# Performance work log

Hardware: AMD Instinct MI355X
Metric: run time of the kernel (lower is better)

## Reference

```python
import jax, jax.numpy as jnp
import numpy as np

N, D, FF, T = 131072, 128, 512, 4
EPS = 1e-5


def layernorm(x, g, b):
    m = jnp.mean(x, axis=-1, keepdims=True)
    v = jnp.mean((x - m) ** 2, axis=-1, keepdims=True)
    return (x - m) * jax.lax.rsqrt(v + EPS) * g + b


def setup_inputs() -> dict:
    key = jax.random.key(0)
    ks = jax.random.split(key, 12)
    s = 1.0 / np.sqrt(D)
    return {
        "x": jax.random.normal(ks[0], (N, D), dtype=jnp.float32),
        # attention projections (single head; nhead=1 is forced by the source's shape constraints)
        "Kw": jax.random.normal(ks[1], (D, D), dtype=jnp.float32) * s,
        "Qw": jax.random.normal(ks[2], (D, D), dtype=jnp.float32) * s,
        "Vw": jax.random.normal(ks[3], (D, D), dtype=jnp.float32) * s,
        "ln1_g": jnp.ones((D,), jnp.float32),
        "ln1_b": jnp.zeros((D,), jnp.float32),
        "ln2_g": jnp.ones((D,), jnp.float32),
        "ln2_b": jnp.zeros((D,), jnp.float32),
        "w1": jax.random.normal(ks[4], (D, FF), dtype=jnp.float32) * s,
        "b1": jnp.zeros((FF,), jnp.float32),
        "w2": jax.random.normal(ks[5], (FF, D), dtype=jnp.float32) / np.sqrt(FF),
        "b2": jnp.zeros((D,), jnp.float32),
        "out_w": jax.random.normal(ks[6], (D, D), dtype=jnp.float32) * s,
        "out_b": jnp.zeros((D,), jnp.float32),
    }


def reference(x, Kw, Qw, Vw, ln1_g, ln1_b, ln2_g, ln2_b, w1, b1, w2, b2, out_w, out_b):
    for _ in range(T):  # same params reused every timestep, as in the source
        # --- softmax-free attention sublayer ---
        h = layernorm(x, ln1_g, ln1_b)
        Q = h @ Qw
        K = h @ Kw
        V = h @ Vw
        # (Q @ K^T) @ V == Q @ (K^T @ V): no softmax, so reassociate to O(n*d^2)
        x = x + Q @ (K.T @ V)
        # --- feed-forward sublayer (Linear-ReLU-Linear implied by dim_ff) ---
        h = layernorm(x, ln2_g, ln2_b)
        x = x + (jax.nn.relu(h @ w1 + b1) @ w2 + b2)
    return x @ out_w + out_b
```

## Files before the change

### kernel.cpp

```cpp
#include <hip/hip_runtime.h>

#define NROWS 131072
#define DIM   128
#define FFD   512
#define TSTEPS 4
#define NBLK  512
#define CHUNK 128
#define NCHUNK 2
#define NSLOT 16
#define SH    136

static_assert((long)NBLK * CHUNK * NCHUNK == NROWS, "grid/chunk mismatch");

typedef short          s8v   __attribute__((ext_vector_type(8)));
typedef float          f4v   __attribute__((ext_vector_type(4)));
typedef unsigned short u16x4 __attribute__((ext_vector_type(4)));

#define MFMA16(a,b,c) __builtin_amdgcn_mfma_f32_16x16x32_bf16((a),(b),(c),0,0,0)

__device__ __forceinline__ unsigned short f2bf(float f){
    unsigned u = __builtin_bit_cast(unsigned, f);
    u += 0x7FFFu + ((u >> 16) & 1u);
    return (unsigned short)(u >> 16);
}
__device__ __forceinline__ float bf2f(unsigned short h){
    return __builtin_bit_cast(float, (unsigned)h << 16);
}
__device__ __forceinline__ f4v ntload4(const float* p){
    return __builtin_nontemporal_load((const f4v*)p);
}
__device__ __forceinline__ void ntstore4(float* p, f4v v){
    __builtin_nontemporal_store(v, (f4v*)p);
}

__global__ __launch_bounds__(512, 2)
void kA(const float* __restrict__ x, const unsigned short* __restrict__ Kwp,
        const unsigned short* __restrict__ Vwp,
        const float* __restrict__ ga, const float* __restrict__ be,
        float* __restrict__ slots)
{
    __shared__ unsigned short hh[128*SH];
    __shared__ unsigned short hl[128*SH];
    __shared__ unsigned short KT[128*SH];
    __shared__ unsigned short VT[128*SH];
    const int tid  = threadIdx.x;
    const int wv   = tid >> 6, lane = tid & 63;
    const int quad = lane >> 4, l15 = lane & 15;
    const int lp   = lane >> 3, lr = lane & 7;
    const int myrow = wv*8 + lr;
    const int pc    = wv*16 + l15;

    s8v bfK[4], bfV[4];
    #pragma unroll
    for (int ks = 0; ks < 4; ++ks) {
        bfK[ks] = *(const s8v*)(Kwp + pc*DIM + ks*32 + quad*8);
        bfV[ks] = *(const s8v*)(Vwp + pc*DIM + ks*32 + quad*8);
    }

    f4v acc[8];
    #pragma unroll
    for (int i = 0; i < 8; ++i) acc[i] = (f4v){0.f,0.f,0.f,0.f};

    for (int ch = 0; ch < NCHUNK; ++ch) {
        const size_t r0 = ((size_t)blockIdx.x*NCHUNK + ch)*CHUNK;
        #pragma unroll
        for (int pp = 0; pp < 2; ++pp) {
            const int row = pp*64 + myrow;
            float v[16];
            #pragma unroll
            for (int j = 0; j < 4; ++j) {
                const f4v t = ntload4(x + (r0 + row)*DIM + lp*16 + j*4);
                v[j*4+0] = t[0]; v[j*4+1] = t[1]; v[j*4+2] = t[2]; v[j*4+3] = t[3];
            }
            float s = 0.f, q = 0.f;
            #pragma unroll
            for (int i = 0; i < 16; ++i) { s += v[i]; q += v[i]*v[i]; }
            #pragma unroll
            for (int o = 8; o < 64; o <<= 1) { s += __shfl_xor(s, o); q += __shfl_xor(q, o); }
            const float m  = s * (1.0f/128.0f);
            const float rs = rsqrtf(q * (1.0f/128.0f) - m*m + 1e-5f);
            unsigned short hi16[16], lo16[16];
            #pragma unroll
            for (int j = 0; j < 4; ++j) {
                const float4 g = *(const float4*)(ga + lp*16 + j*4);
                const float4 b = *(const float4*)(be + lp*16 + j*4);
                float hv0 = (v[j*4+0]-m)*rs*g.x + b.x;
                float hv1 = (v[j*4+1]-m)*rs*g.y + b.y;
                float hv2 = (v[j*4+2]-m)*rs*g.z + b.z;
                float hv3 = (v[j*4+3]-m)*rs*g.w + b.w;
                hi16[j*4+0] = f2bf(hv0); lo16[j*4+0] = f2bf(hv0 - bf2f(hi16[j*4+0]));
                hi16[j*4+1] = f2bf(hv1); lo16[j*4+1] = f2bf(hv1 - bf2f(hi16[j*4+1]));
                hi16[j*4+2] = f2bf(hv2); lo16[j*4+2] = f2bf(hv2 - bf2f(hi16[j*4+2]));
                hi16[j*4+3] = f2bf(hv3); lo16[j*4+3] = f2bf(hv3 - bf2f(hi16[j*4+3]));
            }
            #pragma unroll
            for (int j = 0; j < 2; ++j) {
                *(s8v*)&hh[row*SH + lp*16 + j*8] = *(const s8v*)&hi16[j*8];
                *(s8v*)&hl[row*SH + lp*16 + j*8] = *(const s8v*)&lo16[j*8];
            }
        }
        __syncthreads();
        #pragma unroll
        for (int p = 0; p < 2; ++p) {
            const s8v* bf = p ? bfV : bfK;
            unsigned short* T = p ? VT : KT;
            #pragma unroll
            for (int mt = 0; mt < 8; ++mt) {
                s8v ah[4], al[4];
                #pragma unroll
                for (int ks = 0; ks < 4; ++ks) {
                    ah[ks] = *(const s8v*)(&hh[(mt*16 + l15)*SH + ks*32 + quad*8]);
                    al[ks] = *(const s8v*)(&hl[(mt*16 + l15)*SH + ks*32 + quad*8]);
                }
                f4v c = {0.f,0.f,0.f,0.f};
                #pragma unroll
                for (int ks = 0; ks < 4; ++ks) c = MFMA16(ah[ks], bf[ks], c);
                #pragma unroll
                for (int ks = 0; ks < 4; ++ks) c = MFMA16(al[ks], bf[ks], c);
                u16x4 w4 = { f2bf(c[0]), f2bf(c[1]), f2bf(c[2]), f2bf(c[3]) };
                *(u16x4*)&T[pc*SH + mt*16 + quad*4] = w4;
            }
        }
        __syncthreads();
        #pragma unroll
        for (int ks = 0; ks < 4; ++ks) {
            const s8v af = *(const s8v*)(&KT[pc*SH + ks*32 + quad*8]);
            #pragma unroll
            for (int jt = 0; jt < 8; ++jt) {
                const s8v bfr = *(const s8v*)(&VT[(jt*16 + l15)*SH + ks*32 + quad*8]);
                acc[jt] = MFMA16(af, bfr, acc[jt]);
            }
        }
        __syncthreads();
    }
    float* S = slots + (size_t)(blockIdx.x & (NSLOT-1)) * 16384;
    #pragma unroll
    for (int jt = 0; jt < 8; ++jt) {
        const int i0 = wv*16 + quad*4;
        const int j  = jt*16 + l15;
        #pragma unroll
        for (int rg = 0; rg < 4; ++rg)
            atomicAdd(&S[(i0 + rg)*DIM + j], acc[jt][rg]);
    }
}

__global__ void kReduce(const float* __restrict__ slots, float* __restrict__ ktv)
{
    const int e = blockIdx.x*256 + threadIdx.x;
    float s = 0.f;
    #pragma unroll
    for (int b = 0; b < NSLOT; ++b) s += slots[(size_t)b*16384 + e];
    ktv[e] = s;
}

__global__ void kBuildM(const float* __restrict__ Qw, const float* __restrict__ ktv,
                        unsigned short* __restrict__ Mp, unsigned short* __restrict__ Ml)
{
    const int idx = blockIdx.x*256 + threadIdx.x;
    const int j = idx >> 7, k = idx & 127;
    float s = 0.f;
    for (int i = 0; i < 128; ++i) s += Qw[k*128 + i] * ktv[i*128 + j];
    const unsigned short hi = f2bf(s);
    Mp[idx] = hi;
    Ml[idx] = f2bf(s - bf2f(hi));
}

__global__ __launch_bounds__(512, 2)
void kB(const float* __restrict__ xin, float* __restrict__ xout,
        const unsigned short* __restrict__ Mp, const unsigned short* __restrict__ Ml,
        const float* __restrict__ g1a, const float* __restrict__ b1a,
        const float* __restrict__ g2a, const float* __restrict__ b2a,
        const unsigned short* __restrict__ w1p, const float* __restrict__ fb1,
        const unsigned short* __restrict__ w2p, const float* __restrict__ fb2)
{
    __shared__ float          xb[128*132];
    __shared__ unsigned short hs[128*SH];
    __shared__ unsigned short fbuf[128*SH];
    unsigned short* const hl = fbuf;
    const int tid  = threadIdx.x;
    const int wv   = tid >> 6, lane = tid & 63;
    const int quad = lane >> 4, l15 = lane & 15;
    const int lp   = lane >> 3, lr = lane & 7;
    const int myrow = wv*8 + lr;
    const int cg    = wv*16 + l15;

    s8v bh[4], bl[4];
    #pragma unroll
    for (int ks = 0; ks < 4; ++ks) {
        bh[ks] = *(const s8v*)(Mp + cg*DIM + ks*32 + quad*8);
        bl[ks] = *(const s8v*)(Ml + cg*DIM + ks*32 + quad*8);
    }

    for (int ch = 0; ch < NCHUNK; ++ch) {
        const size_t r0 = ((size_t)blockIdx.x*NCHUNK + ch)*CHUNK;
        #pragma unroll
        for (int i = 0; i < 8; ++i) {
            const int idx = tid + i*512;
            const int r = idx >> 5, c = (idx & 31)*4;
            const f4v t = ntload4(xin + (r0 + r)*DIM + c);
            *(f4v*)&xb[r*132 + c] = t;
        }
        __syncthreads();
        #pragma unroll
        for (int pp = 0; pp < 2; ++pp) {
            const int row = pp*64 + myrow;
            float v[16];
            #pragma unroll
            for (int j = 0; j < 4; ++j)
                *(float4*)&v[j*4] = *(const float4*)&xb[row*132 + lp*16 + j*4];
            float s = 0.f, q = 0.f;
            #pragma unroll
            for (int i = 0; i < 16; ++i) { s += v[i]; q += v[i]*v[i]; }
            #pragma unroll
            for (int o = 8; o < 64; o <<= 1) { s += __shfl_xor(s, o); q += __shfl_xor(q, o); }
            const float m  = s * (1.0f/128.0f);
            const float rs = rsqrtf(q * (1.0f/128.0f) - m*m + 1e-5f);
            unsigned short hi16[16], lo16[16];
            #pragma unroll
            for (int j = 0; j < 4; ++j) {
                const float4 g = *(const float4*)(g1a + lp*16 + j*4);
                const float4 b = *(const float4*)(b1a + lp*16 + j*4);
                float hv0 = (v[j*4+0]-m)*rs*g.x + b.x;
                float hv1 = (v[j*4+1]-m)*rs*g.y + b.y;
                float hv2 = (v[j*4+2]-m)*rs*g.z + b.z;
                float hv3 = (v[j*4+3]-m)*rs*g.w + b.w;
                hi16[j*4+0] = f2bf(hv0); lo16[j*4+0] = f2bf(hv0 - bf2f(hi16[j*4+0]));
                hi16[j*4+1] = f2bf(hv1); lo16[j*4+1] = f2bf(hv1 - bf2f(hi16[j*4+1]));
                hi16[j*4+2] = f2bf(hv2); lo16[j*4+2] = f2bf(hv2 - bf2f(hi16[j*4+2]));
                hi16[j*4+3] = f2bf(hv3); lo16[j*4+3] = f2bf(hv3 - bf2f(hi16[j*4+3]));
            }
            #pragma unroll
            for (int j = 0; j < 2; ++j) {
                *(s8v*)&hs[row*SH + lp*16 + j*8] = *(const s8v*)&hi16[j*8];
                *(s8v*)&hl[row*SH + lp*16 + j*8] = *(const s8v*)&lo16[j*8];
            }
        }
        __syncthreads();
        #pragma unroll
        for (int mt = 0; mt < 8; ++mt) {
            s8v ah[4], al[4];
            #pragma unroll
            for (int ks = 0; ks < 4; ++ks) {
                ah[ks] = *(const s8v*)(&hs[(mt*16 + l15)*SH + ks*32 + quad*8]);
                al[ks] = *(const s8v*)(&hl[(mt*16 + l15)*SH + ks*32 + quad*8]);
            }
            f4v c = {0.f,0.f,0.f,0.f};
            #pragma unroll
            for (int ks = 0; ks < 4; ++ks) c = MFMA16(ah[ks], bh[ks], c);
            #pragma unroll
            for (int ks = 0; ks < 4; ++ks) c = MFMA16(ah[ks], bl[ks], c);
            #pragma unroll
            for (int ks = 0; ks < 4; ++ks) c = MFMA16(al[ks], bh[ks], c);
            #pragma unroll
            for (int rg = 0; rg < 4; ++rg)
                xb[(mt*16 + quad*4 + rg)*132 + cg] += c[rg];
        }
        __syncthreads();
        #pragma unroll
        for (int pp = 0; pp < 2; ++pp) {
            const int row = pp*64 + myrow;
            float v[16];
            #pragma unroll
            for (int j = 0; j < 4; ++j)
                *(float4*)&v[j*4] = *(const float4*)&xb[row*132 + lp*16 + j*4];
            float s = 0.f, q = 0.f;
            #pragma unroll
            for (int i = 0; i < 16; ++i) { s += v[i]; q += v[i]*v[i]; }
            #pragma unroll
            for (int o = 8; o < 64; o <<= 1) { s += __shfl_xor(s, o); q += __shfl_xor(q, o); }
            const float m  = s * (1.0f/128.0f);
            const float rs = rsqrtf(q * (1.0f/128.0f) - m*m + 1e-5f);
            unsigned short hi16[16];
            #pragma unroll
            for (int j = 0; j < 4; ++j) {
                const float4 g = *(const float4*)(g2a + lp*16 + j*4);
                const float4 b = *(const float4*)(b2a + lp*16 + j*4);
                hi16[j*4+0] = f2bf((v[j*4+0]-m)*rs*g.x + b.x);
                hi16[j*4+1] = f2bf((v[j*4+1]-m)*rs*g.y + b.y);
                hi16[j*4+2] = f2bf((v[j*4+2]-m)*rs*g.z + b.z);
                hi16[j*4+3] = f2bf((v[j*4+3]-m)*rs*g.w + b.w);
            }
            #pragma unroll
            for (int j = 0; j < 2; ++j)
                *(s8v*)&hs[row*SH + lp*16 + j*8] = *(const s8v*)&hi16[j*8];
        }
        __syncthreads();
        f4v dx2[8];
        #pragma unroll
        for (int i = 0; i < 8; ++i) dx2[i] = (f4v){0.f,0.f,0.f,0.f};
        #pragma unroll
        for (int qf = 0; qf < 4; ++qf) {
            const int ffc = qf*128 + cg;
            s8v wa[4];
            #pragma unroll
            for (int ks = 0; ks < 4; ++ks)
                wa[ks] = *(const s8v*)(w1p + ffc*DIM + ks*32 + quad*8);
            const float bias = fb1[ffc];
            #pragma unroll
            for (int mt = 0; mt < 8; ++mt) {
                s8v af[4];
                #pragma unroll
                for (int ks = 0; ks < 4; ++ks)
                    af[ks] = *(const s8v*)(&hs[(mt*16 + l15)*SH + ks*32 + quad*8]);
                f4v c = {0.f,0.f,0.f,0.f};
                #pragma unroll
                for (int ks = 0; ks < 4; ++ks) c = MFMA16(af[ks], wa[ks], c);
                #pragma unroll
                for (int rg = 0; rg < 4; ++rg) {
                    float vv = c[rg] + bias;
                    vv = vv > 0.f ? vv : 0.f;
                    fbuf[(mt*16 + quad*4 + rg)*SH + cg] = f2bf(vv);
                }
            }
            __syncthreads();
            s8v wb[4];
            #pragma unroll
            for (int ks = 0; ks < 4; ++ks)
                wb[ks] = *(const s8v*)(w2p + cg*FFD + qf*128 + ks*32 + quad*8);
            #pragma unroll
            for (int mt = 0; mt < 8; ++mt) {
                s8v af[4];
                #pragma unroll
                for (int ks = 0; ks < 4; ++ks)
                    af[ks] = *(const s8v*)(&fbuf[(mt*16 + l15)*SH + ks*32 + quad*8]);
                f4v c = dx2[mt];
                #pragma unroll
                for (int ks = 0; ks < 4; ++ks) c = MFMA16(af[ks], wb[ks], c);
                dx2[mt] = c;
            }
            __syncthreads();
        }
        {
            const float bias = fb2[cg];
            #pragma unroll
            for (int mt = 0; mt < 8; ++mt)
                #pragma unroll
                for (int rg = 0; rg < 4; ++rg)
                    xb[(mt*16 + quad*4 + rg)*132 + cg] += dx2[mt][rg] + bias;
        }
        __syncthreads();
        #pragma unroll
        for (int i = 0; i < 8; ++i) {
            const int idx = tid + i*512;
            const int r = idx >> 5, c = (idx & 31)*4;
            ntstore4(xout + (r0 + r)*DIM + c, *(const f4v*)&xb[r*132 + c]);
        }
        __syncthreads();
    }
}

#define CHUNKF 64
#define NCHUNKF 4
static_assert((long)NBLK * CHUNKF * NCHUNKF == NROWS, "kF grid mismatch");

__global__ __launch_bounds__(256, 2)
void kF(const float* __restrict__ x, const unsigned short* __restrict__ Owp,
        const float* __restrict__ ob, float* __restrict__ out)
{
    __shared__ unsigned short hh[64*SH];
    __shared__ unsigned short hl[64*SH];
    __shared__ float          xb[64*132];
    const int tid  = threadIdx.x;
    const int quad = (tid & 63) >> 4, l15 = tid & 15;
    const int wv_  = tid >> 6;

    s8v bf[2][4];
    #pragma unroll
    for (int nt = 0; nt < 2; ++nt)
        #pragma unroll
        for (int ks = 0; ks < 4; ++ks)
            bf[nt][ks] = *(const s8v*)(Owp + (wv_*32 + nt*16 + l15)*DIM + ks*32 + quad*8);

    for (int ch = 0; ch < NCHUNKF; ++ch) {
        const size_t r0 = ((size_t)blockIdx.x*NCHUNKF + ch)*CHUNKF;
        #pragma unroll
        for (int i = 0; i < 8; ++i) {
            const int idx = tid + i*256;
            const int r = idx >> 5, c = (idx & 31)*4;
            const f4v v = ntload4(x + (r0 + r)*DIM + c);
            const unsigned short h0 = f2bf(v[0]), h1 = f2bf(v[1]),
                                 h2 = f2bf(v[2]), h3 = f2bf(v[3]);
            u16x4 w4 = { h0, h1, h2, h3 };
            u16x4 l4 = { f2bf(v[0] - bf2f(h0)), f2bf(v[1] - bf2f(h1)),
                         f2bf(v[2] - bf2f(h2)), f2bf(v[3] - bf2f(h3)) };
            *(u16x4*)&hh[r*SH + c] = w4;
            *(u16x4*)&hl[r*SH + c] = l4;
        }
        __syncthreads();
        #pragma unroll
        for (int mt = 0; mt < 4; ++mt) {
            s8v ah[4], al[4];
            #pragma unroll
            for (int ks = 0; ks < 4; ++ks) {
                ah[ks] = *(const s8v*)(&hh[(mt*16 + l15)*SH + ks*32 + quad*8]);
                al[ks] = *(const s8v*)(&hl[(mt*16 + l15)*SH + ks*32 + quad*8]);
            }
            #pragma unroll
            for (int nt = 0; nt < 2; ++nt) {
                f4v c = {0.f,0.f,0.f,0.f};
                #pragma unroll
                for (int ks = 0; ks < 4; ++ks) c = MFMA16(ah[ks], bf[nt][ks], c);
                #pragma unroll
                for (int ks = 0; ks < 4; ++ks) c = MFMA16(al[ks], bf[nt][ks], c);
                const int cg = wv_*32 + nt*16 + l15;
                const float bias = ob[cg];
                #pragma unroll
                for (int rg = 0; rg < 4; ++rg)
                    xb[(mt*16 + quad*4 + rg)*132 + cg] = c[rg] + bias;
            }
        }
        __syncthreads();
        #pragma unroll
        for (int i = 0; i < 8; ++i) {
            const int idx = tid + i*256;
            const int r = idx >> 5, c = (idx & 31)*4;
            ntstore4(out + (r0 + r)*DIM + c, *(const f4v*)&xb[r*132 + c]);
        }
        __syncthreads();
    }
}

__global__ void kPack(const float* __restrict__ Kw, const float* __restrict__ Vw,
                      const float* __restrict__ Ow, const float* __restrict__ w1,
                      const float* __restrict__ w2,
                      unsigned short* __restrict__ Kwp, unsigned short* __restrict__ Vwp,
                      unsigned short* __restrict__ Owp, unsigned short* __restrict__ w1p,
                      unsigned short* __restrict__ w2p)
{
    const int t = blockIdx.x*256 + threadIdx.x;
    if (t < 16384) {
        const int n = t >> 7, k = t & 127;
        Kwp[t] = f2bf(Kw[k*128 + n]);
        Vwp[t] = f2bf(Vw[k*128 + n]);
        Owp[t] = f2bf(Ow[k*128 + n]);
    } else if (t < 16384 + 65536) {
        const int u = t - 16384;
        const int n = u >> 7, k = u & 127;
        w1p[u] = f2bf(w1[k*FFD + n]);
    } else {
        const int u = t - 16384 - 65536;
        const int n = u >> 9, k = u & 511;
        w2p[u] = f2bf(w2[k*DIM + n]);
    }
}

extern "C" void kernel_launch(void* const* d_in, const int* in_sizes, int n_in,
                              void* d_out, int out_size, void* d_ws, size_t ws_size,
                              hipStream_t stream)
{
    (void)in_sizes; (void)n_in; (void)out_size; (void)ws_size;
    const float* x_in = (const float*)d_in[0];
    const float* Kw   = (const float*)d_in[1];
    const float* Qw   = (const float*)d_in[2];
    const float* Vw   = (const float*)d_in[3];
    const float* ln1g = (const float*)d_in[4];
    const float* ln1b = (const float*)d_in[5];
    const float* ln2g = (const float*)d_in[6];
    const float* ln2b = (const float*)d_in[7];
    const float* w1   = (const float*)d_in[8];
    const float* b1   = (const float*)d_in[9];
    const float* w2   = (const float*)d_in[10];
    const float* b2   = (const float*)d_in[11];
    const float* Ow   = (const float*)d_in[12];
    const float* ob   = (const float*)d_in[13];

    char* p = (char*)d_ws;
    float* slots        = (float*)p;          p += (size_t)NSLOT*16384*4;
    float* ktv          = (float*)p;          p += 16384*4;
    unsigned short* Kwp = (unsigned short*)p; p += 16384*2;
    unsigned short* Vwp = (unsigned short*)p; p += 16384*2;
    unsigned short* Owp = (unsigned short*)p; p += 16384*2;
    unsigned short* w1p = (unsigned short*)p; p += 65536*2;
    unsigned short* w2p = (unsigned short*)p; p += 65536*2;
    unsigned short* Mp  = (unsigned short*)p; p += 16384*2;
    unsigned short* Ml  = (unsigned short*)p; p += 16384*2;

    float* X = (float*)d_out;

    kPack<<<576, 256, 0, stream>>>(Kw, Vw, Ow, w1, w2, Kwp, Vwp, Owp, w1p, w2p);

    const float* src = x_in;
    for (int t = 0; t < TSTEPS; ++t) {
        hipMemsetAsync(slots, 0, (size_t)NSLOT*16384*4, stream);
        kA<<<NBLK, 512, 0, stream>>>(src, Kwp, Vwp, ln1g, ln1b, slots);
        kReduce<<<64, 256, 0, stream>>>(slots, ktv);
        kBuildM<<<64, 256, 0, stream>>>(Qw, ktv, Mp, Ml);
        kB<<<NBLK, 512, 0, stream>>>(src, X, Mp, Ml, ln1g, ln1b, ln2g, ln2b,
                                     w1p, b1, w2p, b2);
        src = X;
    }
    kF<<<NBLK, 256, 0, stream>>>(X, Owp, ob, (float*)d_out);
}
```

Measured before the change: 1.195 ms.

## Fuse next-step K^T·V accumulation into block kernel and final projection into last step

The per-row block kernel now does two more things after writing the updated x. It recomputes LayerNorm1 on the rows it already holds in LDS, projects them through K and V with MFMA, and accumulates the next timestep's K^T·V into the slot buffer with atomics. This removes the separate kA pass, and its full read of x, for steps 2 to 4. The last timestep uses a separate variant that applies the output projection directly, which removes the standalone kF pass. In exchange, LDS is aliased across more phases, the per-block epilogue gets longer, and more register pressure is added from the persistent accumulators.

```diff
diff --git a/kernel.cpp b/kernel.cpp
--- a/kernel.cpp
+++ b/kernel.cpp
@@ -166,17 +166,23 @@
 }
 
 __global__ __launch_bounds__(512, 2)
-void kB(const float* __restrict__ xin, float* __restrict__ xout,
-        const unsigned short* __restrict__ Mp, const unsigned short* __restrict__ Ml,
-        const float* __restrict__ g1a, const float* __restrict__ b1a,
-        const float* __restrict__ g2a, const float* __restrict__ b2a,
-        const unsigned short* __restrict__ w1p, const float* __restrict__ fb1,
-        const unsigned short* __restrict__ w2p, const float* __restrict__ fb2)
+void kBmid(const float* __restrict__ xin, float* __restrict__ xout,
+           const unsigned short* __restrict__ Mp, const unsigned short* __restrict__ Ml,
+           const float* __restrict__ g1a, const float* __restrict__ b1a,
+           const float* __restrict__ g2a, const float* __restrict__ b2a,
+           const unsigned short* __restrict__ w1p, const float* __restrict__ fb1,
+           const unsigned short* __restrict__ w2p, const float* __restrict__ fb2,
+           const unsigned short* __restrict__ Kwp, const unsigned short* __restrict__ Vwp,
+           float* __restrict__ slots)
 {
-    __shared__ float          xb[128*132];
-    __shared__ unsigned short hs[128*SH];
-    __shared__ unsigned short fbuf[128*SH];
-    unsigned short* const hl = fbuf;
+    __shared__ __align__(16) char lds_raw[139264];
+    unsigned short* const hs = (unsigned short*)lds_raw;
+    unsigned short* const hl = (unsigned short*)(lds_raw + 34816);
+    float*          const xb = (float*)(lds_raw + 69632);
+    unsigned short* const KT = (unsigned short*)(lds_raw + 69632);
+    unsigned short* const VT = (unsigned short*)(lds_raw + 104448);
+    unsigned short* const fbuf = hl;
+
     const int tid  = threadIdx.x;
     const int wv   = tid >> 6, lane = tid & 63;
     const int quad = lane >> 4, l15 = lane & 15;
@@ -184,12 +190,9 @@
     const int myrow = wv*8 + lr;
     const int cg    = wv*16 + l15;
 
-    s8v bh[4], bl[4];
+    f4v acc[8];
     #pragma unroll
-    for (int ks = 0; ks < 4; ++ks) {
-        bh[ks] = *(const s8v*)(Mp + cg*DIM + ks*32 + quad*8);
-        bl[ks] = *(const s8v*)(Ml + cg*DIM + ks*32 + quad*8);
-    }
+    for (int i = 0; i < 8; ++i) acc[i] = (f4v){0.f,0.f,0.f,0.f};
 
     for (int ch = 0; ch < NCHUNK; ++ch) {
         const size_t r0 = ((size_t)blockIdx.x*NCHUNK + ch)*CHUNK;
@@ -236,24 +239,32 @@
             }
         }
         __syncthreads();
-        #pragma unroll
-        for (int mt = 0; mt < 8; ++mt) {
-            s8v ah[4], al[4];
+        {
+            s8v bh[4], bl[4];
             #pragma unroll
             for (int ks = 0; ks < 4; ++ks) {
-                ah[ks] = *(const s8v*)(&hs[(mt*16 + l15)*SH + ks*32 + quad*8]);
-                al[ks] = *(const s8v*)(&hl[(mt*16 + l15)*SH + ks*32 + quad*8]);
-            }
-            f4v c = {0.f,0.f,0.f,0.f};
-            #pragma unroll
-            for (int ks = 0; ks < 4; ++ks) c = MFMA16(ah[ks], bh[ks], c);
-            #pragma unroll
-            for (int ks = 0; ks < 4; ++ks) c = MFMA16(ah[ks], bl[ks], c);
-            #pragma unroll
-            for (int ks = 0; ks < 4; ++ks) c = MFMA16(al[ks], bh[ks], c);
-            #pragma unroll
-            for (int rg = 0; rg < 4; ++rg)
-                xb[(mt*16 + quad*4 + rg)*132 + cg] += c[rg];
+                bh[ks] = *(const s8v*)(Mp + cg*DIM + ks*32 + quad*8);
+                bl[ks] = *(const s8v*)(Ml + cg*DIM + ks*32 + quad*8);
+            }
+            #pragma unroll
+            for (int mt = 0; mt < 8; ++mt) {
+                s8v ah[4], al[4];
+                #pragma unroll
+                for (int ks = 0; ks < 4; ++ks) {
+                    ah[ks] = *(const s8v*)(&hs[(mt*16 + l15)*SH + ks*32 + quad*8]);
+                    al[ks] = *(const s8v*)(&hl[(mt*16 + l15)*SH + ks*32 + quad*8]);
+                }
+                f4v c = {0.f,0.f,0.f,0.f};
+                #pragma unroll
+                for (int ks = 0; ks < 4; ++ks) c = MFMA16(ah[ks], bh[ks], c);
+                #pragma unroll
+                for (int ks = 0; ks < 4; ++ks) c = MFMA16(ah[ks], bl[ks], c);
+                #pragma unroll
+                for (int ks = 0; ks < 4; ++ks) c = MFMA16(al[ks], bh[ks], c);
+                #pragma unroll
+                for (int rg = 0; rg < 4; ++rg)
+                    xb[(mt*16 + quad*4 + rg)*132 + cg] += c[rg];
+            }
         }
         __syncthreads();
         #pragma unroll
@@ -345,65 +356,303 @@
             const int r = idx >> 5, c = (idx & 31)*4;
             ntstore4(xout + (r0 + r)*DIM + c, *(const f4v*)&xb[r*132 + c]);
         }
+        #pragma unroll
+        for (int pp = 0; pp < 2; ++pp) {
+            const int row = pp*64 + myrow;
+            float v[16];
+            #pragma unroll
+            for (int j = 0; j < 4; ++j)
+                *(float4*)&v[j*4] = *(const float4*)&xb[row*132 + lp*16 + j*4];
+            float s = 0.f, q = 0.f;
+            #pragma unroll
+            for (int i = 0; i < 16; ++i) { s += v[i]; q += v[i]*v[i]; }
+            #pragma unroll
+            for (int o = 8; o < 64; o <<= 1) { s += __shfl_xor(s, o); q += __shfl_xor(q, o); }
+            const float m  = s * (1.0f/128.0f);
+            const float rs = rsqrtf(q * (1.0f/128.0f) - m*m + 1e-5f);
+            unsigned short hi16[16], lo16[16];
+            #pragma unroll
+            for (int j = 0; j < 4; ++j) {
+                const float4 g = *(const float4*)(g1a + lp*16 + j*4);
+                const float4 b = *(const float4*)(b1a + lp*16 + j*4);
+                float hv0 = (v[j*4+0]-m)*rs*g.x + b.x;
+                float hv1 = (v[j*4+1]-m)*rs*g.y + b.y;
+                float hv2 = (v[j*4+2]-m)*rs*g.z + b.z;
+                float hv3 = (v[j*4+3]-m)*rs*g.w + b.w;
+                hi16[j*4+0] = f2bf(hv0); lo16[j*4+0] = f2bf(hv0 - bf2f(hi16[j*4+0]));
+                hi16[j*4+1] = f2bf(hv1); lo16[j*4+1] = f2bf(hv1 - bf2f(hi16[j*4+1]));
+                hi16[j*4+2] = f2bf(hv2); lo16[j*4+2] = f2bf(hv2 - bf2f(hi16[j*4+2]));
+                hi16[j*4+3] = f2bf(hv3); lo16[j*4+3] = f2bf(hv3 - bf2f(hi16[j*4+3]));
+            }
+            #pragma unroll
+            for (int j = 0; j < 2; ++j) {
+                *(s8v*)&hs[row*SH + lp*16 + j*8] = *(const s8v*)&hi16[j*8];
+                *(s8v*)&hl[row*SH + lp*16 + j*8] = *(const s8v*)&lo16[j*8];
+            }
+        }
+        __syncthreads();
+        {
+            s8v bfK[4], bfV[4];
+            #pragma unroll
+            for (int ks = 0; ks < 4; ++ks) {
+                bfK[ks] = *(const s8v*)(Kwp + cg*DIM + ks*32 + quad*8);
+                bfV[ks] = *(const s8v*)(Vwp + cg*DIM + ks*32 + quad*8);
+            }
+            #pragma unroll
+            for (int p = 0; p < 2; ++p) {
+                const s8v* bf = p ? bfV : bfK;
+                unsigned short* T = p ? VT : KT;
+                #pragma unroll
+                for (int mt = 0; mt < 8; ++mt) {
+                    s8v ah[4], al[4];
+                    #pragma unroll
+                    for (int ks = 0; ks < 4; ++ks) {
+                        ah[ks] = *(const s8v*)(&hs[(mt*16 + l15)*SH + ks*32 + quad*8]);
+                        al[ks] = *(const s8v*)(&hl[(mt*16 + l15)*SH + ks*32 + quad*8]);
+                    }
+                    f4v c = {0.f,0.f,0.f,0.f};
+                    #pragma unroll
+                    for (int ks = 0; ks < 4; ++ks) c = MFMA16(ah[ks], bf[ks], c);
+                    #pragma unroll
+                    for (int ks = 0; ks < 4; ++ks) c = MFMA16(al[ks], bf[ks], c);
+                    u16x4 w4 = { f2bf(c[0]), f2bf(c[1]), f2bf(c[2]), f2bf(c[3]) };
+                    *(u16x4*)&T[cg*SH + mt*16 + quad*4] = w4;
+                }
+            }
+        }
+        __syncthreads();
+        #pragma unroll
+        for (int ks = 0; ks < 4; ++ks) {
+            const s8v af = *(const s8v*)(&KT[cg*SH + ks*32 + quad*8]);
+            #pragma unroll
+            for (int jt = 0; jt < 8; ++jt) {
+                const s8v bfr = *(const s8v*)(&VT[(jt*16 + l15)*SH + ks*32 + quad*8]);
+                acc[jt] = MFMA16(af, bfr, acc[jt]);
+            }
+        }
         __syncthreads();
     }
-}
-
-#define CHUNKF 64
-#define NCHUNKF 4
-static_assert((long)NBLK * CHUNKF * NCHUNKF == NROWS, "kF grid mismatch");
-
-__global__ __launch_bounds__(256, 2)
-void kF(const float* __restrict__ x, const unsigned short* __restrict__ Owp,
-        const float* __restrict__ ob, float* __restrict__ out)
+    float* S = slots + (size_t)(blockIdx.x & (NSLOT-1)) * 16384;
+    #pragma unroll
+    for (int jt = 0; jt < 8; ++jt) {
+        const int i0 = wv*16 + quad*4;
+        const int j  = jt*16 + l15;
+        #pragma unroll
+        for (int rg = 0; rg < 4; ++rg)
+            atomicAdd(&S[(i0 + rg)*DIM + j], acc[jt][rg]);
+    }
+}
+
+__global__ __launch_bounds__(512, 2)
+void kBlast(const float* __restrict__ xin,
+            const unsigned short* __restrict__ Mp, const unsigned short* __restrict__ Ml,
+            const float* __restrict__ g1a, const float* __restrict__ b1a,
+            const float* __restrict__ g2a, const float* __restrict__ b2a,
+            const unsigned short* __restrict__ w1p, const float* __restrict__ fb1,
+            const unsigned short* __restrict__ w2p, const float* __restrict__ fb2,
+            const unsigned short* __restrict__ Owp, const float* __restrict__ ob,
+            float* __restrict__ out)
 {
-    __shared__ unsigned short hh[64*SH];
-    __shared__ unsigned short hl[64*SH];
-    __shared__ float          xb[64*132];
+    __shared__ unsigned short hs[128*SH];
+    __shared__ unsigned short fbuf[128*SH];
+    __shared__ float          xb[128*132];
+    unsigned short* const hl = fbuf;
     const int tid  = threadIdx.x;
-    const int quad = (tid & 63) >> 4, l15 = tid & 15;
-    const int wv_  = tid >> 6;
-
-    s8v bf[2][4];
-    #pragma unroll
-    for (int nt = 0; nt < 2; ++nt)
-        #pragma unroll
-        for (int ks = 0; ks < 4; ++ks)
-            bf[nt][ks] = *(const s8v*)(Owp + (wv_*32 + nt*16 + l15)*DIM + ks*32 + quad*8);
-
-    for (int ch = 0; ch < NCHUNKF; ++ch) {
-        const size_t r0 = ((size_t)blockIdx.x*NCHUNKF + ch)*CHUNKF;
+    const int wv   = tid >> 6, lane = tid & 63;
+    const int quad = lane >> 4, l15 = lane & 15;
+    const int lp   = lane >> 3, lr = lane & 7;
+    const int myrow = wv*8 + lr;
+    const int cg    = wv*16 + l15;
+
+    for (int ch = 0; ch < NCHUNK; ++ch) {
+        const size_t r0 = ((size_t)blockIdx.x*NCHUNK + ch)*CHUNK;
         #pragma unroll
         for (int i = 0; i < 8; ++i) {
-            const int idx = tid + i*256;
+            const int idx = tid + i*512;
             const int r = idx >> 5, c = (idx & 31)*4;
-            const f4v v = ntload4(x + (r0 + r)*DIM + c);
-            const unsigned short h0 = f2bf(v[0]), h1 = f2bf(v[1]),
-                                 h2 = f2bf(v[2]), h3 = f2bf(v[3]);
+            const f4v t = ntload4(xin + (r0 + r)*DIM + c);
+            *(f4v*)&xb[r*132 + c] = t;
+        }
+        __syncthreads();
+        #pragma unroll
+        for (int pp = 0; pp < 2; ++pp) {
+            const int row = pp*64 + myrow;
+            float v[16];
+            #pragma unroll
+            for (int j = 0; j < 4; ++j)
+                *(float4*)&v[j*4] = *(const float4*)&xb[row*132 + lp*16 + j*4];
+            float s = 0.f, q = 0.f;
+            #pragma unroll
+            for (int i = 0; i < 16; ++i) { s += v[i]; q += v[i]*v[i]; }
+            #pragma unroll
+            for (int o = 8; o < 64; o <<= 1) { s += __shfl_xor(s, o); q += __shfl_xor(q, o); }
+            const float m  = s * (1.0f/128.0f);
+            const float rs = rsqrtf(q * (1.0f/128.0f) - m*m + 1e-5f);
+            unsigned short hi16[16], lo16[16];
+            #pragma unroll
+            for (int j = 0; j < 4; ++j) {
+                const float4 g = *(const float4*)(g1a + lp*16 + j*4);
+                const float4 b = *(const float4*)(b1a + lp*16 + j*4);
+                float hv0 = (v[j*4+0]-m)*rs*g.x + b.x;
+                float hv1 = (v[j*4+1]-m)*rs*g.y + b.y;
+                float hv2 = (v[j*4+2]-m)*rs*g.z + b.z;
+                float hv3 = (v[j*4+3]-m)*rs*g.w + b.w;
+                hi16[j*4+0] = f2bf(hv0); lo16[j*4+0] = f2bf(hv0 - bf2f(hi16[j*4+0]));
+                hi16[j*4+1] = f2bf(hv1); lo16[j*4+1] = f2bf(hv1 - bf2f(hi16[j*4+1]));
+                hi16[j*4+2] = f2bf(hv2); lo16[j*4+2] = f2bf(hv2 - bf2f(hi16[j*4+2]));
+                hi16[j*4+3] = f2bf(hv3); lo16[j*4+3] = f2bf(hv3 - bf2f(hi16[j*4+3]));
+            }
+            #pragma unroll
+            for (int j = 0; j < 2; ++j) {
+                *(s8v*)&hs[row*SH + lp*16 + j*8] = *(const s8v*)&hi16[j*8];
+                *(s8v*)&hl[row*SH + lp*16 + j*8] = *(const s8v*)&lo16[j*8];
+            }
+        }
+        __syncthreads();
+        {
+            s8v bh[4], bl[4];
+            #pragma unroll
+            for (int ks = 0; ks < 4; ++ks) {
+                bh[ks] = *(const s8v*)(Mp + cg*DIM + ks*32 + quad*8);
+                bl[ks] = *(const s8v*)(Ml + cg*DIM + ks*32 + quad*8);
+            }
+            #pragma unroll
+            for (int mt = 0; mt < 8; ++mt) {
+                s8v ah[4], al[4];
+                #pragma unroll
+                for (int ks = 0; ks < 4; ++ks) {
+                    ah[ks] = *(const s8v*)(&hs[(mt*16 + l15)*SH + ks*32 + quad*8]);
+                    al[ks] = *(const s8v*)(&hl[(mt*16 + l15)*SH + ks*32 + quad*8]);
+                }
+                f4v c = {0.f,0.f,0.f,0.f};
+                #pragma unroll
+                for (int ks = 0; ks < 4; ++ks) c = MFMA16(ah[ks], bh[ks], c);
+                #pragma unroll
+                for (int ks = 0; ks < 4; ++ks) c = MFMA16(ah[ks], bl[ks], c);
+                #pragma unroll
+                for (int ks = 0; ks < 4; ++ks) c = MFMA16(al[ks], bh[ks], c);
+                #pragma unroll
+                for (int rg = 0; rg < 4; ++rg)
+                    xb[(mt*16 + quad*4 + rg)*132 + cg] += c[rg];
+            }
+        }
+        __syncthreads();
+        #pragma unroll
+        for (int pp = 0; pp < 2; ++pp) {
+            const int row = pp*64 + myrow;
+            float v[16];
+            #pragma unroll
+            for (int j = 0; j < 4; ++j)
+                *(float4*)&v[j*4] = *(const float4*)&xb[row*132 + lp*16 + j*4];
+            float s = 0.f, q = 0.f;
+            #pragma unroll
+            for (int i = 0; i < 16; ++i) { s += v[i]; q += v[i]*v[i]; }
+            #pragma unroll
+            for (int o = 8; o < 64; o <<= 1) { s += __shfl_xor(s, o); q += __shfl_xor(q, o); }
+            const float m  = s * (1.0f/128.0f);
+            const float rs = rsqrtf(q * (1.0f/128.0f) - m*m + 1e-5f);
+            unsigned short hi16[16];
+            #pragma unroll
+            for (int j = 0; j < 4; ++j) {
+                const float4 g = *(const float4*)(g2a + lp*16 + j*4);
+                const float4 b = *(const float4*)(b2a + lp*16 + j*4);
+                hi16[j*4+0] = f2bf((v[j*4+0]-m)*rs*g.x + b.x);
+                hi16[j*4+1] = f2bf((v[j*4+1]-m)*rs*g.y + b.y);
+                hi16[j*4+2] = f2bf((v[j*4+2]-m)*rs*g.z + b.z);
+                hi16[j*4+3] = f2bf((v[j*4+3]-m)*rs*g.w + b.w);
+            }
+            #pragma unroll
+            for (int j = 0; j < 2; ++j)
+                *(s8v*)&hs[row*SH + lp*16 + j*8] = *(const s8v*)&hi16[j*8];
+        }
+        __syncthreads();
+        f4v dx2[8];
+        #pragma unroll
+        for (int i = 0; i < 8; ++i) dx2[i] = (f4v){0.f,0.f,0.f,0.f};
+        #pragma unroll
+        for (int qf = 0; qf < 4; ++qf) {
+            const int ffc = qf*128 + cg;
+            s8v wa[4];
+            #pragma unroll
+            for (int ks = 0; ks < 4; ++ks)
+                wa[ks] = *(const s8v*)(w1p + ffc*DIM + ks*32 + quad*8);
+            const float bias = fb1[ffc];
+            #pragma unroll
+            for (int mt = 0; mt < 8; ++mt) {
+                s8v af[4];
+                #pragma unroll
+                for (int ks = 0; ks < 4; ++ks)
+                    af[ks] = *(const s8v*)(&hs[(mt*16 + l15)*SH + ks*32 + quad*8]);
+                f4v c = {0.f,0.f,0.f,0.f};
+                #pragma unroll
+                for (int ks = 0; ks < 4; ++ks) c = MFMA16(af[ks], wa[ks], c);
+                #pragma unroll
+                for (int rg = 0; rg < 4; ++rg) {
+                    float vv = c[rg] + bias;
+                    vv = vv > 0.f ? vv : 0.f;
+                    fbuf[(mt*16 + quad*4 + rg)*SH + cg] = f2bf(vv);
+                }
+            }
+            __syncthreads();
+            s8v wb[4];
+            #pragma unroll
+            for (int ks = 0; ks < 4; ++ks)
+                wb[ks] = *(const s8v*)(w2p + cg*FFD + qf*128 + ks*32 + quad*8);
+            #pragma unroll
+            for (int mt = 0; mt < 8; ++mt) {
+                s8v af[4];
+                #pragma unroll
+                for (int ks = 0; ks < 4; ++ks)
+                    af[ks] = *(const s8v*)(&fbuf[(mt*16 + l15)*SH + ks*32 + quad*8]);
+                f4v c = dx2[mt];
+                #pragma unroll
+                for (int ks = 0; ks < 4; ++ks) c = MFMA16(af[ks], wb[ks], c);
+                dx2[mt] = c;
+            }
+            __syncthreads();
+        }
+        {
+            const float bias = fb2[cg];
+            #pragma unroll
+            for (int mt = 0; mt < 8; ++mt)
+                #pragma unroll
+                for (int rg = 0; rg < 4; ++rg)
+                    xb[(mt*16 + quad*4 + rg)*132 + cg] += dx2[mt][rg] + bias;
+        }
+        __syncthreads();
+        #pragma unroll
+        for (int i = 0; i < 8; ++i) {
+            const int idx = tid + i*512;
+            const int r = idx >> 5, c = (idx & 31)*4;
+            const float4 v = *(const float4*)&xb[r*132 + c];
+            const unsigned short h0 = f2bf(v.x), h1 = f2bf(v.y),
+                                 h2 = f2bf(v.z), h3 = f2bf(v.w);
             u16x4 w4 = { h0, h1, h2, h3 };
-            u16x4 l4 = { f2bf(v[0] - bf2f(h0)), f2bf(v[1] - bf2f(h1)),
-                         f2bf(v[2] - bf2f(h2)), f2bf(v[3] - bf2f(h3)) };
-            *(u16x4*)&hh[r*SH + c] = w4;
+            u16x4 l4 = { f2bf(v.x - bf2f(h0)), f2bf(v.y - bf2f(h1)),
+                         f2bf(v.z - bf2f(h2)), f2bf(v.w - bf2f(h3)) };
+            *(u16x4*)&hs[r*SH + c] = w4;
             *(u16x4*)&hl[r*SH + c] = l4;
         }
         __syncthreads();
-        #pragma unroll
-        for (int mt = 0; mt < 4; ++mt) {
-            s8v ah[4], al[4];
-            #pragma unroll
-            for (int ks = 0; ks < 4; ++ks) {
-                ah[ks] = *(const s8v*)(&hh[(mt*16 + l15)*SH + ks*32 + quad*8]);
-                al[ks] = *(const s8v*)(&hl[(mt*16 + l15)*SH + ks*32 + quad*8]);
-            }
-            #pragma unroll
-            for (int nt = 0; nt < 2; ++nt) {
+        {
+            s8v bfO[4];
+            #pragma unroll
+            for (int ks = 0; ks < 4; ++ks)
+                bfO[ks] = *(const s8v*)(Owp + cg*DIM + ks*32 + quad*8);
+            const float bias = ob[cg];
+            #pragma unroll
+            for (int mt = 0; mt < 8; ++mt) {
+                s8v ah[4], al[4];
+                #pragma unroll
+                for (int ks = 0; ks < 4; ++ks) {
+                    ah[ks] = *(const s8v*)(&hs[(mt*16 + l15)*SH + ks*32 + quad*8]);
+                    al[ks] = *(const s8v*)(&hl[(mt*16 + l15)*SH + ks*32 + quad*8]);
+                }
                 f4v c = {0.f,0.f,0.f,0.f};
                 #pragma unroll
-                for (int ks = 0; ks < 4; ++ks) c = MFMA16(ah[ks], bf[nt][ks], c);
-                #pragma unroll
-                for (int ks = 0; ks < 4; ++ks) c = MFMA16(al[ks], bf[nt][ks], c);
-                const int cg = wv_*32 + nt*16 + l15;
-                const float bias = ob[cg];
+                for (int ks = 0; ks < 4; ++ks) c = MFMA16(ah[ks], bfO[ks], c);
+                #pragma unroll
+                for (int ks = 0; ks < 4; ++ks) c = MFMA16(al[ks], bfO[ks], c);
                 #pragma unroll
                 for (int rg = 0; rg < 4; ++rg)
                     xb[(mt*16 + quad*4 + rg)*132 + cg] = c[rg] + bias;
@@ -412,7 +661,7 @@
         __syncthreads();
         #pragma unroll
         for (int i = 0; i < 8; ++i) {
-            const int idx = tid + i*256;
+            const int idx = tid + i*512;
             const int r = idx >> 5, c = (idx & 31)*4;
             ntstore4(out + (r0 + r)*DIM + c, *(const f4v*)&xb[r*132 + c]);
         }
@@ -479,15 +728,20 @@
 
     kPack<<<576, 256, 0, stream>>>(Kw, Vw, Ow, w1, w2, Kwp, Vwp, Owp, w1p, w2p);
 
+    (void)hipMemsetAsync(slots, 0, (size_t)NSLOT*16384*4, stream);
+    kA<<<NBLK, 512, 0, stream>>>(x_in, Kwp, Vwp, ln1g, ln1b, slots);
+
     const float* src = x_in;
-    for (int t = 0; t < TSTEPS; ++t) {
-        hipMemsetAsync(slots, 0, (size_t)NSLOT*16384*4, stream);
-        kA<<<NBLK, 512, 0, stream>>>(src, Kwp, Vwp, ln1g, ln1b, slots);
+    for (int t = 0; t < TSTEPS-1; ++t) {
         kReduce<<<64, 256, 0, stream>>>(slots, ktv);
         kBuildM<<<64, 256, 0, stream>>>(Qw, ktv, Mp, Ml);
-        kB<<<NBLK, 512, 0, stream>>>(src, X, Mp, Ml, ln1g, ln1b, ln2g, ln2b,
-                                     w1p, b1, w2p, b2);
+        (void)hipMemsetAsync(slots, 0, (size_t)NSLOT*16384*4, stream);
+        kBmid<<<NBLK, 512, 0, stream>>>(src, X, Mp, Ml, ln1g, ln1b, ln2g, ln2b,
+                                        w1p, b1, w2p, b2, Kwp, Vwp, slots);
         src = X;
     }
-    kF<<<NBLK, 256, 0, stream>>>(X, Owp, ob, (float*)d_out);
-}
+    kReduce<<<64, 256, 0, stream>>>(slots, ktv);
+    kBuildM<<<64, 256, 0, stream>>>(Qw, ktv, Mp, Ml);
+    kBlast<<<NBLK, 512, 0, stream>>>(src, Mp, Ml, ln1g, ln1b, ln2g, ln2b,
+                                     w1p, b1, w2p, b2, Owp, ob, (float*)d_out);
+}
```

Result: slower. 1.233 ms (+3.2%).
